# Kernel optimization log

Measured on AMD Instinct MI355X. Metric: run time of the kernel, lower is better.

## Reference

```python
import jax, jax.numpy as jnp
import numpy as np

GAMMA = 1.0

C, K, D = 10000, 4, 2048  # classes, prototypes per class, feature dim


def setup_inputs() -> dict:
    key = jax.random.key(0)
    k1, k2 = jax.random.split(key)
    feature = jax.random.normal(k1, (D,), dtype=jnp.float32)
    all_prototypes = jax.random.normal(k2, (C, K, D), dtype=jnp.float32)
    label = 7
    return {"feature": feature, "label": label, "all_prototypes": all_prototypes}


def reference(feature, label, all_prototypes):
    # squared euclidean distance from feature to every prototype: [C, K]
    diff = all_prototypes - feature  # broadcast [C,K,D]
    d = jnp.sum(diff * diff, axis=-1)  # [C,K]
    logits = -GAMMA * d  # [C,K]
    # denominator: one = sum_{c,k} exp(-gamma * d_{c,k}); use stable logsumexp
    log_one = jax.nn.logsumexp(logits)
    # probability = sum_k -log(exp(logits[label,k]) / one)
    #             = sum_k (gamma * d[label,k] + log(one))
    lbl_logits = jax.lax.dynamic_index_in_dim(logits, label, axis=0, keepdims=False)  # [K]
    probability = jnp.sum(log_one - lbl_logits)
    return probability
```

## Files before the change

kernel.cpp:

```cpp
#include <hip/hip_runtime.h>

#define C_CLASSES 10000
#define K_PROTO   4
#define D_DIM     2048
#define ROWS      (C_CLASSES * K_PROTO)
#define D_VEC     (D_DIM / 4)
#define RPW       4
#define NBLOCKS   2500
#define NWAVES    (NBLOCKS * 4)

typedef float v4f __attribute__((ext_vector_type(4)));

__global__ __launch_bounds__(256) void dist_kernel(const v4f* __restrict__ proto,
                                                   const v4f* __restrict__ feat,
                                                   const int* __restrict__ label,
                                                   float2* __restrict__ wave_pair,
                                                   float* __restrict__ d_label) {
    const int wave = (blockIdx.x << 2) | (threadIdx.x >> 6);
    const int lane = threadIdx.x & 63;
    const int lbl  = label[0];
    const v4f* p0  = proto + (size_t)wave * RPW * D_VEC;

    v4f f[8];
#pragma unroll
    for (int j = 0; j < 8; ++j) f[j] = feat[j * 64 + lane];

    v4f r[RPW][8];
#pragma unroll
    for (int rr = 0; rr < RPW; ++rr)
#pragma unroll
        for (int j = 0; j < 8; ++j)
            r[rr][j] = __builtin_nontemporal_load(&p0[rr * D_VEC + j * 64 + lane]);

    float acc[RPW];
#pragma unroll
    for (int rr = 0; rr < RPW; ++rr) {
        float a = 0.0f;
#pragma unroll
        for (int j = 0; j < 8; ++j) {
            const float dx = r[rr][j].x - f[j].x;
            const float dy = r[rr][j].y - f[j].y;
            const float dz = r[rr][j].z - f[j].z;
            const float dw = r[rr][j].w - f[j].w;
            a += dx * dx + dy * dy + dz * dz + dw * dw;
        }
        acc[rr] = a;
    }

#pragma unroll
    for (int m = 1; m <= 2; m <<= 1) {
        acc[0] += __shfl_xor(acc[0], m, 64);
        acc[1] += __shfl_xor(acc[1], m, 64);
        acc[2] += __shfl_xor(acc[2], m, 64);
        acc[3] += __shfl_xor(acc[3], m, 64);
    }
    const int l3 = lane & 3;
    float v = acc[0];
    v = (l3 == 1) ? acc[1] : v;
    v = (l3 == 2) ? acc[2] : v;
    v = (l3 == 3) ? acc[3] : v;
#pragma unroll
    for (int m = 4; m <= 32; m <<= 1) v += __shfl_xor(v, m, 64);

    float mn = fminf(v, __shfl_xor(v, 1, 64));
    mn = fminf(mn, __shfl_xor(mn, 2, 64));
    float s = expf(mn - v);
    s += __shfl_xor(s, 1, 64);
    s += __shfl_xor(s, 2, 64);

    if (lane == 0) wave_pair[wave] = make_float2(mn, s);
    if (wave == lbl && lane < 4) d_label[lane] = v;
}

__global__ __launch_bounds__(1024) void finalize_kernel(const float4* __restrict__ pairs4,
                                                        const float* __restrict__ d_label,
                                                        float* __restrict__ out) {
    __shared__ float sm[20];
    const int tid  = threadIdx.x;
    const int lane = tid & 63;
    const int wid  = tid >> 6;
    const int N4   = NWAVES / 2;

    float m = 3.402823466e38f;
    for (int i = tid; i < N4; i += 1024) {
        const float4 p = pairs4[i];
        m = fminf(m, fminf(p.x, p.z));
    }
#pragma unroll
    for (int off = 1; off < 64; off <<= 1) m = fminf(m, __shfl_xor(m, off, 64));
    if (lane == 0) sm[wid] = m;
    __syncthreads();
    if (tid == 0) {
        float mm = sm[0];
#pragma unroll
        for (int i = 1; i < 16; ++i) mm = fminf(mm, sm[i]);
        sm[16] = mm;
    }
    __syncthreads();
    const float dmin = sm[16];

    float acc = 0.0f;
    for (int i = tid; i < N4; i += 1024) {
        const float4 p = pairs4[i];
        acc += p.y * expf(dmin - p.x) + p.w * expf(dmin - p.z);
    }
#pragma unroll
    for (int off = 1; off < 64; off <<= 1) acc += __shfl_xor(acc, off, 64);
    if (lane == 0) sm[wid] = acc;
    __syncthreads();
    if (tid == 0) {
        float ss = 0.0f;
#pragma unroll
        for (int i = 0; i < 16; ++i) ss += sm[i];
        const float log_one = -dmin + logf(ss);
        float p = 0.0f;
#pragma unroll
        for (int k = 0; k < K_PROTO; ++k) p += log_one + d_label[k];
        out[0] = p;
    }
}

extern "C" void kernel_launch(void* const* d_in, const int* in_sizes, int n_in,
                              void* d_out, int out_size, void* d_ws, size_t ws_size,
                              hipStream_t stream) {
    const float* feat  = (const float*)d_in[0];
    const int*   label = (const int*)d_in[1];
    const float* proto = (const float*)d_in[2];
    float* out = (float*)d_out;

    float2* wave_pair = (float2*)d_ws;
    float*  d_label   = (float*)(wave_pair + NWAVES);

    dist_kernel<<<NBLOCKS, 256, 0, stream>>>(
        (const v4f*)proto, (const v4f*)feat, label, wave_pair, d_label);
    finalize_kernel<<<1, 1024, 0, stream>>>((const float4*)wave_pair, d_label, out);
}
```

Baseline: 408.3 us.

## Process four classes per wave with double-buffered row loads, defer softmax to finalize

Each wave now handles 16 prototype rows (four classes) instead of 4, streaming them through a two-slot register double buffer so the next row's loads are issued while the current row is reduced. The grid shrinks to 625 blocks. The per-wave min/exp partial logsumexp is dropped; all 40000 distances are written out and the finalize kernel does the full min and exp-sum over them, and also reads the label distances. The aim is better latency hiding with fewer waves, at the cost of lower occupancy and a heavier single-block finalize (40000 exps instead of 10000 pairs).

```diff
diff --git a/kernel.cpp b/kernel.cpp
--- a/kernel.cpp
+++ b/kernel.cpp
@@ -5,86 +5,84 @@
 #define D_DIM     2048
 #define ROWS      (C_CLASSES * K_PROTO)
 #define D_VEC     (D_DIM / 4)
-#define RPW       4
-#define NBLOCKS   2500
-#define NWAVES    (NBLOCKS * 4)
+#define CPW       4
+#define NBLOCKS   625
 
 typedef float v4f __attribute__((ext_vector_type(4)));
 
 __global__ __launch_bounds__(256) void dist_kernel(const v4f* __restrict__ proto,
                                                    const v4f* __restrict__ feat,
-                                                   const int* __restrict__ label,
-                                                   float2* __restrict__ wave_pair,
-                                                   float* __restrict__ d_label) {
+                                                   float* __restrict__ d_all) {
     const int wave = (blockIdx.x << 2) | (threadIdx.x >> 6);
     const int lane = threadIdx.x & 63;
-    const int lbl  = label[0];
-    const v4f* p0  = proto + (size_t)wave * RPW * D_VEC;
+    const v4f* p0  = proto + (size_t)wave * CPW * K_PROTO * D_VEC;
 
     v4f f[8];
 #pragma unroll
     for (int j = 0; j < 8; ++j) f[j] = feat[j * 64 + lane];
 
-    v4f r[RPW][8];
+    v4f buf[2][8];
 #pragma unroll
-    for (int rr = 0; rr < RPW; ++rr)
-#pragma unroll
-        for (int j = 0; j < 8; ++j)
-            r[rr][j] = __builtin_nontemporal_load(&p0[rr * D_VEC + j * 64 + lane]);
-
-    float acc[RPW];
-#pragma unroll
-    for (int rr = 0; rr < RPW; ++rr) {
-        float a = 0.0f;
-#pragma unroll
-        for (int j = 0; j < 8; ++j) {
-            const float dx = r[rr][j].x - f[j].x;
-            const float dy = r[rr][j].y - f[j].y;
-            const float dz = r[rr][j].z - f[j].z;
-            const float dw = r[rr][j].w - f[j].w;
-            a += dx * dx + dy * dy + dz * dz + dw * dw;
-        }
-        acc[rr] = a;
-    }
+    for (int j = 0; j < 8; ++j)
+        buf[0][j] = __builtin_nontemporal_load(&p0[j * 64 + lane]);
 
 #pragma unroll
-    for (int m = 1; m <= 2; m <<= 1) {
-        acc[0] += __shfl_xor(acc[0], m, 64);
-        acc[1] += __shfl_xor(acc[1], m, 64);
-        acc[2] += __shfl_xor(acc[2], m, 64);
-        acc[3] += __shfl_xor(acc[3], m, 64);
+    for (int c = 0; c < CPW; ++c) {
+        float acc[4];
+#pragma unroll
+        for (int rr = 0; rr < 4; ++rr) {
+            const int rg = c * 4 + rr;
+            if (rg + 1 < CPW * 4) {
+                const v4f* pn = p0 + (size_t)(rg + 1) * D_VEC;
+#pragma unroll
+                for (int j = 0; j < 8; ++j)
+                    buf[(rg + 1) & 1][j] = __builtin_nontemporal_load(&pn[j * 64 + lane]);
+            }
+            const v4f* cur = buf[rg & 1];
+            float a = 0.0f;
+#pragma unroll
+            for (int j = 0; j < 8; ++j) {
+                const float dx = cur[j].x - f[j].x;
+                const float dy = cur[j].y - f[j].y;
+                const float dz = cur[j].z - f[j].z;
+                const float dw = cur[j].w - f[j].w;
+                a += dx * dx + dy * dy + dz * dz + dw * dw;
+            }
+            acc[rr] = a;
+        }
+
+#pragma unroll
+        for (int m = 1; m <= 2; m <<= 1) {
+            acc[0] += __shfl_xor(acc[0], m, 64);
+            acc[1] += __shfl_xor(acc[1], m, 64);
+            acc[2] += __shfl_xor(acc[2], m, 64);
+            acc[3] += __shfl_xor(acc[3], m, 64);
+        }
+        const int l3 = lane & 3;
+        float v = acc[0];
+        v = (l3 == 1) ? acc[1] : v;
+        v = (l3 == 2) ? acc[2] : v;
+        v = (l3 == 3) ? acc[3] : v;
+#pragma unroll
+        for (int m = 4; m <= 32; m <<= 1) v += __shfl_xor(v, m, 64);
+
+        if (lane < 4) d_all[(size_t)(wave * CPW + c) * 4 + lane] = v;
     }
-    const int l3 = lane & 3;
-    float v = acc[0];
-    v = (l3 == 1) ? acc[1] : v;
-    v = (l3 == 2) ? acc[2] : v;
-    v = (l3 == 3) ? acc[3] : v;
-#pragma unroll
-    for (int m = 4; m <= 32; m <<= 1) v += __shfl_xor(v, m, 64);
-
-    float mn = fminf(v, __shfl_xor(v, 1, 64));
-    mn = fminf(mn, __shfl_xor(mn, 2, 64));
-    float s = expf(mn - v);
-    s += __shfl_xor(s, 1, 64);
-    s += __shfl_xor(s, 2, 64);
-
-    if (lane == 0) wave_pair[wave] = make_float2(mn, s);
-    if (wave == lbl && lane < 4) d_label[lane] = v;
 }
 
-__global__ __launch_bounds__(1024) void finalize_kernel(const float4* __restrict__ pairs4,
-                                                        const float* __restrict__ d_label,
+__global__ __launch_bounds__(1024) void finalize_kernel(const float4* __restrict__ d4,
+                                                        const int* __restrict__ label,
                                                         float* __restrict__ out) {
     __shared__ float sm[20];
     const int tid  = threadIdx.x;
     const int lane = tid & 63;
     const int wid  = tid >> 6;
-    const int N4   = NWAVES / 2;
+    const int N4   = ROWS / 4;
 
     float m = 3.402823466e38f;
     for (int i = tid; i < N4; i += 1024) {
-        const float4 p = pairs4[i];
-        m = fminf(m, fminf(p.x, p.z));
+        const float4 p = d4[i];
+        m = fminf(m, fminf(fminf(p.x, p.y), fminf(p.z, p.w)));
     }
 #pragma unroll
     for (int off = 1; off < 64; off <<= 1) m = fminf(m, __shfl_xor(m, off, 64));
@@ -101,8 +99,9 @@
 
     float acc = 0.0f;
     for (int i = tid; i < N4; i += 1024) {
-        const float4 p = pairs4[i];
-        acc += p.y * expf(dmin - p.x) + p.w * expf(dmin - p.z);
+        const float4 p = d4[i];
+        acc += expf(dmin - p.x) + expf(dmin - p.y) +
+               expf(dmin - p.z) + expf(dmin - p.w);
     }
 #pragma unroll
     for (int off = 1; off < 64; off <<= 1) acc += __shfl_xor(acc, off, 64);
@@ -113,9 +112,11 @@
 #pragma unroll
         for (int i = 0; i < 16; ++i) ss += sm[i];
         const float log_one = -dmin + logf(ss);
+        const float* d_all = (const float*)d4;
+        const int lbl = label[0];
         float p = 0.0f;
 #pragma unroll
-        for (int k = 0; k < K_PROTO; ++k) p += log_one + d_label[k];
+        for (int k = 0; k < K_PROTO; ++k) p += log_one + d_all[lbl * K_PROTO + k];
         out[0] = p;
     }
 }
@@ -126,12 +127,10 @@
     const float* feat  = (const float*)d_in[0];
     const int*   label = (const int*)d_in[1];
     const float* proto = (const float*)d_in[2];
-    float* out = (float*)d_out;
-
-    float2* wave_pair = (float2*)d_ws;
-    float*  d_label   = (float*)(wave_pair + NWAVES);
+    float* out   = (float*)d_out;
+    float* d_all = (float*)d_ws;
 
     dist_kernel<<<NBLOCKS, 256, 0, stream>>>(
-        (const v4f*)proto, (const v4f*)feat, label, wave_pair, d_label);
-    finalize_kernel<<<1, 1024, 0, stream>>>((const float4*)wave_pair, d_label, out);
+        (const v4f*)proto, (const v4f*)feat, d_all);
+    finalize_kernel<<<1, 1024, 0, stream>>>((const float4*)d_all, label, out);
 }
```

Result: slower. 419.9 us (+2.8%).
